# Kernel optimization log

Measured on AMD Instinct MI355X. Metric: run time of the kernel, lower is better.

The kernel has to match this reference:

```python
import jax, jax.numpy as jnp
import numpy as np

NUM_EMBEDDINGS = 8192
EMBEDDING_DIM = 256
COMMITMENT_COST = 0.25


def setup_inputs() -> dict:
    key = jax.random.key(0)
    k1, k2 = jax.random.split(key)
    inputs = jax.random.normal(k1, (32, EMBEDDING_DIM, 1024), dtype=jnp.float32)
    # matches nn.Embedding init: uniform(-1/K, 1/K)
    scale = 1.0 / NUM_EMBEDDINGS
    weight = jax.random.uniform(k2, (NUM_EMBEDDINGS, EMBEDDING_DIM),
                                minval=-scale, maxval=scale, dtype=jnp.float32)
    return {"inputs": inputs, "weight": weight}


def reference(inputs, weight):
    # inputs: [B, D, T] -> [B, T, D]
    x = jnp.transpose(inputs, (0, 2, 1))
    B, T, D = x.shape
    flat = x.reshape(-1, D)  # [N, D]
    # squared-L2 distances to each codeword: [N, K]
    distances = (jnp.sum(flat ** 2, axis=1, keepdims=True)
                 + jnp.sum(weight ** 2, axis=1)
                 - 2.0 * flat @ weight.T)
    encoding_indices = jnp.argmin(distances, axis=1)  # [N]
    # one-hot @ weight is just a gather
    quantized = weight[encoding_indices].reshape(x.shape)  # [B, T, D]
    # straight-through estimator
    quantized_ste = x + jax.lax.stop_gradient(quantized - x)
    e_latent_loss = jnp.mean((jax.lax.stop_gradient(quantized_ste) - x) ** 2)
    q_latent_loss = jnp.mean((quantized_ste - jax.lax.stop_gradient(x)) ** 2)
    loss = q_latent_loss + COMMITMENT_COST * e_latent_loss
    quantized_out = jnp.transpose(quantized_ste, (0, 2, 1))  # [B, D, T]
    return loss, quantized_out, encoding_indices[:, None]
```

## Files before the change

### kernel.cpp

```cpp
#include <hip/hip_runtime.h>
#include <hip/hip_bf16.h>

#define Bn 32
#define Dd 256
#define Tt 1024
#define Nn (Bn * Tt)
#define Kk 8192

typedef __attribute__((ext_vector_type(8))) short bf16x8;
typedef __attribute__((ext_vector_type(4))) float f32x4;

static __device__ __forceinline__ short f2bf(float v) {
    __hip_bfloat16 h = __float2bfloat16(v);
    return *reinterpret_cast<short*>(&h);
}

#define OFF_XT    0ULL
#define OFF_XBT   33554432ULL
#define OFF_WBT   50331648ULL
#define OFF_CM    54525952ULL
#define OFF_LIST  71303168ULL
#define OFF_KEYS  75497472ULL
#define OFF_SW2   75759616ULL
#define OFF_CN    75792384ULL
#define OFF_CNT   75923456ULL
#define OFF_PART  75923712ULL
#define WS_NEED   75927808ULL
#define OFF_MASK  OFF_XBT

__global__ void k_xprep(const float* __restrict__ x, float* __restrict__ xT,
                        short* __restrict__ xbt) {
    __shared__ float tile[32][33];
    const int b = blockIdx.z, d0 = blockIdx.y * 32, t0 = blockIdx.x * 32;
    const int tx = threadIdx.x, ty = threadIdx.y;
#pragma unroll
    for (int r = 0; r < 32; r += 8)
        tile[ty + r][tx] = x[((size_t)(b * Dd + d0 + ty + r)) * Tt + t0 + tx];
    __syncthreads();
#pragma unroll
    for (int r = 0; r < 32; r += 8) {
        const size_t o = (size_t)(b * Tt + t0 + ty + r) * Dd + d0 + tx;
        const float v = tile[tx][ty + r];
        xT[o] = v;
        xbt[o] = f2bf(v);
    }
}

__global__ void k_wbf(const float* __restrict__ w, short* __restrict__ wbt) {
    const int i = (blockIdx.x * 256 + threadIdx.x) * 4;
    const float4 v = *reinterpret_cast<const float4*>(&w[i]);
    short4 o;
    o.x = f2bf(v.x); o.y = f2bf(v.y); o.z = f2bf(v.z); o.w = f2bf(v.w);
    *reinterpret_cast<short4*>(&wbt[i]) = o;
}

__global__ void k_sumx2_np(const float* __restrict__ x, float* __restrict__ c) {
#pragma clang fp contract(off)
    const int n = blockIdx.x * 256 + threadIdx.x;
    const int b = n >> 10, t = n & 1023;
    const float* p = x + (size_t)b * (Dd * Tt) + t;
    float h[2];
#pragma unroll
    for (int half = 0; half < 2; ++half) {
        float r[8];
#pragma unroll
        for (int j = 0; j < 8; ++j) {
            const float v = p[(size_t)(half * 128 + j) * Tt];
            r[j] = v * v;
        }
        for (int i = 8; i < 128; i += 8) {
#pragma unroll
            for (int j = 0; j < 8; ++j) {
                const float v = p[(size_t)(half * 128 + i + j) * Tt];
                const float sq = v * v;
                r[j] = r[j] + sq;
            }
        }
        h[half] = ((r[0] + r[1]) + (r[2] + r[3])) + ((r[4] + r[5]) + (r[6] + r[7]));
    }
    c[n] = h[0] + h[1];
}

__global__ void k_sumw2_np(const float* __restrict__ w, float* __restrict__ sw) {
#pragma clang fp contract(off)
    const int k = blockIdx.x * 256 + threadIdx.x;
    const float* p = w + (size_t)k * Dd;
    float h[2];
#pragma unroll
    for (int half = 0; half < 2; ++half) {
        float r[8];
#pragma unroll
        for (int j = 0; j < 8; ++j) {
            const float v = p[half * 128 + j];
            r[j] = v * v;
        }
        for (int i = 8; i < 128; i += 8) {
#pragma unroll
            for (int j = 0; j < 8; ++j) {
                const float v = p[half * 128 + i + j];
                const float sq = v * v;
                r[j] = r[j] + sq;
            }
        }
        h[half] = ((r[0] + r[1]) + (r[2] + r[3])) + ((r[4] + r[5]) + (r[6] + r[7]));
    }
    sw[k] = h[0] + h[1];
}

__global__ void __launch_bounds__(512, 4)
k_mfma_filter(const short* __restrict__ xbt, const short* __restrict__ wbt,
              const float* __restrict__ sw2, float* __restrict__ cm) {
    __shared__ __align__(16) short Ws[128 * 264];
    const int tid = threadIdx.x;
    const int n0 = blockIdx.x * 128;
    const int cbase = blockIdx.y * 32;
    const int wid = tid >> 6, lane = tid & 63;
    const int rp = wid >> 1, cp = wid & 1;
    const int l15 = lane & 15, l4 = lane >> 4;

    bf16x8 a[2][8];
#pragma unroll
    for (int rt = 0; rt < 2; ++rt)
#pragma unroll
        for (int ks = 0; ks < 8; ++ks)
            a[rt][ks] = *reinterpret_cast<const bf16x8*>(
                &xbt[(size_t)(n0 + 32 * rp + 16 * rt + l15) * Dd + 32 * ks + 8 * l4]);

    for (int cc = 0; cc < 32; ++cc) {
        const int c = cbase + cc;
#pragma unroll
        for (int m = 0; m < 8; ++m) {
            const int e = tid + 512 * m;
            const int code = e >> 5, d8 = e & 31;
            *reinterpret_cast<bf16x8*>(&Ws[code * 264 + 8 * d8]) =
                *reinterpret_cast<const bf16x8*>(
                    &wbt[(size_t)(128 * c + code) * Dd + 8 * d8]);
        }
        __syncthreads();

        f32x4 acc[2][4];
#pragma unroll
        for (int rt = 0; rt < 2; ++rt)
#pragma unroll
            for (int ct = 0; ct < 4; ++ct) acc[rt][ct] = (f32x4)0.0f;

#pragma unroll
        for (int ks = 0; ks < 8; ++ks) {
            bf16x8 b[4];
#pragma unroll
            for (int ct = 0; ct < 4; ++ct)
                b[ct] = *reinterpret_cast<const bf16x8*>(
                    &Ws[(64 * cp + 16 * ct + l15) * 264 + 32 * ks + 8 * l4]);
#pragma unroll
            for (int rt = 0; rt < 2; ++rt)
#pragma unroll
                for (int ct = 0; ct < 4; ++ct)
                    acc[rt][ct] = __builtin_amdgcn_mfma_f32_16x16x32_bf16(
                        a[rt][ks], b[ct], acc[rt][ct], 0, 0, 0);
        }
        __syncthreads();

        float swc[4];
#pragma unroll
        for (int ct = 0; ct < 4; ++ct)
            swc[ct] = sw2[128 * c + 64 * cp + 16 * ct + l15];
#pragma unroll
        for (int rt = 0; rt < 2; ++rt) {
#pragma unroll
            for (int r = 0; r < 4; ++r) {
                float mm = fmaf(-2.0f, acc[rt][0][r], swc[0]);
#pragma unroll
                for (int ct = 1; ct < 4; ++ct)
                    mm = fminf(mm, fmaf(-2.0f, acc[rt][ct][r], swc[ct]));
#pragma unroll
                for (int d = 1; d < 16; d <<= 1)
                    mm = fminf(mm, __shfl_xor(mm, d));
                if (l15 == 0) {
                    const int row = n0 + 32 * rp + 16 * rt + 4 * l4 + r;
                    cm[(size_t)row * 128 + 2 * c + cp] = mm;
                }
            }
        }
    }
}

__global__ void __launch_bounds__(256)
k_mask(const float* __restrict__ cm, const float* __restrict__ cn,
       unsigned long long* __restrict__ mask, unsigned long long* __restrict__ keys) {
    const int tid = threadIdx.x;
    const int lane = tid & 63, w = tid >> 6;
    const int grp = lane >> 4, sub = lane & 15;
    const int n0 = blockIdx.x * 256;
    for (int pass = 0; pass < 16; ++pass) {
        const int row = n0 + pass * 16 + 4 * w + grp;
        const float4 v0 = *reinterpret_cast<const float4*>(&cm[(size_t)row * 128 + 8 * sub]);
        const float4 v1 = *reinterpret_cast<const float4*>(&cm[(size_t)row * 128 + 8 * sub + 4]);
        float gmin = fminf(fminf(fminf(v0.x, v0.y), fminf(v0.z, v0.w)),
                           fminf(fminf(v1.x, v1.y), fminf(v1.z, v1.w)));
#pragma unroll
        for (int m = 1; m < 16; m <<= 1) gmin = fminf(gmin, __shfl_xor(gmin, m));
        const float margin = 7.1e-5f + 2.6e-5f * sqrtf(cn[row]);
        const float thr = gmin + margin;
        unsigned int nib = 0;
        if (fminf(v0.x, v0.y) <= thr) nib |= 1u;
        if (fminf(v0.z, v0.w) <= thr) nib |= 2u;
        if (fminf(v1.x, v1.y) <= thr) nib |= 4u;
        if (fminf(v1.z, v1.w) <= thr) nib |= 8u;
        unsigned long long mk = (unsigned long long)nib << (4 * sub);
#pragma unroll
        for (int m = 1; m < 16; m <<= 1) mk |= __shfl_xor(mk, m);
        if (sub == 0) {
            mask[row] = mk;
            keys[row] = 0xFFFFFFFFFFFFFFFFULL;
        }
    }
}

__global__ void __launch_bounds__(1024)
k_compact(const unsigned long long* __restrict__ mask,
          unsigned int* __restrict__ cnt, unsigned short* __restrict__ lists) {
    __shared__ unsigned int sc[1024];
    const int c = blockIdx.x;
    const int t = threadIdx.x;
    const int r0 = t * 32;
    unsigned int word = 0;
#pragma unroll
    for (int j = 0; j < 32; ++j)
        word |= (unsigned int)((mask[r0 + j] >> c) & 1ULL) << j;
    const unsigned int mycnt = __popc(word);
    sc[t] = mycnt;
    __syncthreads();
    for (int off = 1; off < 1024; off <<= 1) {
        const unsigned int v = sc[t];
        const unsigned int add = (t >= off) ? sc[t - off] : 0u;
        __syncthreads();
        sc[t] = v + add;
        __syncthreads();
    }
    unsigned int base = sc[t] - mycnt;
    unsigned short* lc = lists + (size_t)c * Nn;
    unsigned int wrd = word;
    while (wrd) {
        const int j = __ffs(wrd) - 1;
        lc[base++] = (unsigned short)(r0 + j);
        wrd &= wrd - 1;
    }
    if (t == 1023) cnt[c] = sc[1023];
}

#define NGB 8
__global__ void __launch_bounds__(256, 1)
k_refine(const float* __restrict__ xT, const float* __restrict__ w,
         const float* __restrict__ sw2, const float* __restrict__ cn,
         const unsigned int* __restrict__ cnt, const unsigned short* __restrict__ lists,
         unsigned long long* __restrict__ keys) {
    __shared__ __align__(16) float xs[64 * 260];
    __shared__ __align__(16) float ws[128 * 68];
    __shared__ float cns[64];
    __shared__ unsigned short rid_s[64];
    const int c = blockIdx.x, gb = blockIdx.y;
    const int tid = threadIdx.x;
    const int cntc = (int)cnt[c];
    const int kl = tid & 31, rg = tid >> 5;
    float swk[4];
#pragma unroll
    for (int cc = 0; cc < 4; ++cc) swk[cc] = sw2[128 * c + kl + 32 * cc];

    for (int start = gb * 64; start < cntc; start += NGB * 64) {
#pragma unroll
        for (int m = 0; m < 16; ++m) {
            const int e = tid + 256 * m;
            const int j = e >> 6, d4 = e & 63;
            const int li = min(start + j, cntc - 1);
            const int row = lists[(size_t)c * Nn + li];
            *reinterpret_cast<float4*>(&xs[j * 260 + 4 * d4]) =
                *reinterpret_cast<const float4*>(&xT[(size_t)row * Dd + 4 * d4]);
        }
        if (tid < 64) {
            const int li = min(start + tid, cntc - 1);
            const unsigned short row = lists[(size_t)c * Nn + li];
            rid_s[tid] = row;
            cns[tid] = cn[row];
        }
        __syncthreads();

        float acc[8][4];
#pragma unroll
        for (int rr = 0; rr < 8; ++rr)
#pragma unroll
            for (int cc = 0; cc < 4; ++cc) acc[rr][cc] = 0.0f;

        for (int step = 0; step < 4; ++step) {
#pragma unroll
            for (int m = 0; m < 8; ++m) {
                const int e = tid + 256 * m;
                const int code = e >> 4, dseg = e & 15;
                *reinterpret_cast<float4*>(&ws[code * 68 + 4 * dseg]) =
                    *reinterpret_cast<const float4*>(
                        &w[(size_t)(128 * c + code) * Dd + step * 64 + 4 * dseg]);
            }
            __syncthreads();
#pragma unroll
            for (int dl = 0; dl < 16; ++dl) {
                float4 wv[4];
#pragma unroll
                for (int cc = 0; cc < 4; ++cc)
                    wv[cc] = *reinterpret_cast<const float4*>(
                        &ws[(kl + 32 * cc) * 68 + 4 * dl]);
#pragma unroll
                for (int rr = 0; rr < 8; ++rr) {
                    const float4 xv = *reinterpret_cast<const float4*>(
                        &xs[(8 * rg + rr) * 260 + step * 64 + 4 * dl]);
#pragma unroll
                    for (int cc = 0; cc < 4; ++cc) {
                        acc[rr][cc] = fmaf(xv.x, wv[cc].x, acc[rr][cc]);
                        acc[rr][cc] = fmaf(xv.y, wv[cc].y, acc[rr][cc]);
                        acc[rr][cc] = fmaf(xv.z, wv[cc].z, acc[rr][cc]);
                        acc[rr][cc] = fmaf(xv.w, wv[cc].w, acc[rr][cc]);
                    }
                }
            }
            __syncthreads();
        }

#pragma unroll
        for (int rr = 0; rr < 8; ++rr) {
            const int rl = 8 * rg + rr;
            const float cr = cns[rl];
            float bv = 3.402823466e+38f;
            int bk = 0x7FFFFFFF;
#pragma unroll
            for (int cc = 0; cc < 4; ++cc) {
                const float t1 = cr + swk[cc];
                const float s = fmaf(-2.0f, acc[rr][cc], t1);
                const int k = 128 * c + kl + 32 * cc;
                if (s < bv || (s == bv && k < bk)) { bv = s; bk = k; }
            }
#pragma unroll
            for (int d = 1; d < 32; d <<= 1) {
                const float ov = __shfl_xor(bv, d);
                const int ok = __shfl_xor(bk, d);
                if (ov < bv || (ov == bv && ok < bk)) { bv = ov; bk = ok; }
            }
            if (kl == 0) {
                const unsigned long long key =
                    ((unsigned long long)__float_as_uint(bv) << 32) |
                    (unsigned long long)(unsigned int)bk;
                atomicMin(&keys[rid_s[rl]], key);
            }
        }
        __syncthreads();
    }
}

__global__ void k_quant2(const float* __restrict__ x, const float* __restrict__ w,
                         const unsigned long long* __restrict__ keys,
                         float* __restrict__ outq, float* __restrict__ idxf,
                         double* __restrict__ part) {
#pragma clang fp contract(off)
    __shared__ double red[256];
    const int tid = threadIdx.x;
    const int n0 = blockIdx.x * 64;
    const int b = n0 >> 10, t0 = n0 & 1023;
    const int tl = tid & 63;
    const int d0 = tid >> 6;
    const int n = n0 + tl;
    const int code = (int)(unsigned int)(keys[n] & 0xFFFFFFFFULL);
    if (tid < 64) idxf[n0 + tid] = (float)(int)(unsigned int)(keys[n0 + tid] & 0xFFFFFFFFULL);
    const float* wr = w + (size_t)code * Dd;
    const size_t base = (size_t)b * (Dd * Tt) + t0 + tl;
    double s = 0.0;
    for (int d = d0; d < Dd; d += 4) {
        const float xv = x[base + (size_t)d * Tt];
        const float qv = wr[d];
        const float d1 = qv - xv;
        const float qs = xv + d1;
        const float d2 = qs - xv;
        s += (double)d2 * (double)d2;
        outq[base + (size_t)d * Tt] = qs;
    }
    red[tid] = s;
    __syncthreads();
    for (int st = 128; st > 0; st >>= 1) {
        if (tid < st) red[tid] += red[tid + st];
        __syncthreads();
    }
    if (tid == 0) part[blockIdx.x] = red[0];
}

__global__ void k_loss(const double* __restrict__ part, float* __restrict__ loss) {
    __shared__ double red[512];
    const int tid = threadIdx.x;
    red[tid] = part[tid];
    __syncthreads();
    for (int st = 256; st > 0; st >>= 1) {
        if (tid < st) red[tid] += red[tid + st];
        __syncthreads();
    }
    if (tid == 0)
        loss[0] = (float)(1.25 * red[0] / (double)((size_t)Bn * Dd * Tt));
}

__global__ void k_transpose(const float* __restrict__ w, float* __restrict__ wtg) {
    __shared__ float tile[32][33];
    const int k0 = blockIdx.x * 32;
    const int d0 = blockIdx.y * 32;
    const int tx = threadIdx.x, ty = threadIdx.y;
#pragma unroll
    for (int r = 0; r < 32; r += 8)
        tile[r + ty][tx] = w[(size_t)(k0 + r + ty) * Dd + d0 + tx];
    __syncthreads();
#pragma unroll
    for (int r = 0; r < 32; r += 8)
        wtg[(size_t)(d0 + r + ty) * Kk + k0 + tx] = tile[tx][r + ty];
}

template <bool WTG>
__global__ void __launch_bounds__(512, 2)
k_argmin(const float* __restrict__ x, const float* __restrict__ w,
         const float* __restrict__ wtg, const float* __restrict__ sw2,
         const float* __restrict__ cn,
         int* __restrict__ idx_out, float* __restrict__ idx_f) {
    __shared__ __align__(16) float At[32][132];
    __shared__ __align__(16) float Wt[32][268];
    const int tid = threadIdx.x;
    const int n0 = blockIdx.x * 128;
    const int b = n0 >> 10;
    const int t0 = n0 & 1023;
    const int ty = tid >> 5;
    const int tx = tid & 31;
    const int r0 = ty * 4;
    const int c0 = tx * 4;
    const float* xb = x + (size_t)b * (Dd * Tt) + t0;

    float c8[8];
#pragma unroll
    for (int i = 0; i < 8; ++i) {
        const int row = (i < 4) ? (r0 + i) : (64 + r0 + (i - 4));
        c8[i] = cn[n0 + row];
    }
    float best[8];
    int bidx[8];
#pragma unroll
    for (int i = 0; i < 8; ++i) { best[i] = 3.402823466e+38f; bidx[i] = 0; }

    for (int kc = 0; kc < Kk; kc += 256) {
        float acc[8][8];
#pragma unroll
        for (int i = 0; i < 8; ++i)
#pragma unroll
            for (int j = 0; j < 8; ++j) acc[i][j] = 0.0f;
        for (int ds = 0; ds < Dd; ds += 32) {
#pragma unroll
            for (int u = 0; u < 2; ++u) {
                int cc = tid + 512 * u;
                int dd = cc >> 5, i4 = cc & 31;
                float4 v = *reinterpret_cast<const float4*>(
                    &xb[(size_t)(ds + dd) * Tt + i4 * 4]);
                *reinterpret_cast<float4*>(&At[dd][i4 * 4]) = v;
            }
            if (WTG) {
#pragma unroll
                for (int u = 0; u < 4; ++u) {
                    int cc = tid + 512 * u;
                    int dd = cc >> 6, j4 = cc & 63;
                    float4 v = *reinterpret_cast<const float4*>(
                        &wtg[(size_t)(ds + dd) * Kk + kc + j4 * 4]);
                    *reinterpret_cast<float4*>(&Wt[dd][j4 * 4]) = v;
                }
            } else {
#pragma unroll
                for (int u = 0; u < 4; ++u) {
                    int cc = tid + 512 * u;
                    int j = cc >> 3, m = cc & 7;
                    float4 v = *reinterpret_cast<const float4*>(
                        &w[(size_t)(kc + j) * Dd + ds + m * 4]);
                    Wt[m * 4 + 0][j] = v.x;
                    Wt[m * 4 + 1][j] = v.y;
                    Wt[m * 4 + 2][j] = v.z;
                    Wt[m * 4 + 3][j] = v.w;
                }
            }
            __syncthreads();
#pragma unroll 8
            for (int dd = 0; dd < 32; ++dd) {
                float4 a0 = *reinterpret_cast<const float4*>(&At[dd][r0]);
                float4 a1 = *reinterpret_cast<const float4*>(&At[dd][64 + r0]);
                float4 b0 = *reinterpret_cast<const float4*>(&Wt[dd][c0]);
                float4 b1 = *reinterpret_cast<const float4*>(&Wt[dd][128 + c0]);
                float av[8] = {a0.x, a0.y, a0.z, a0.w, a1.x, a1.y, a1.z, a1.w};
                float bv[8] = {b0.x, b0.y, b0.z, b0.w, b1.x, b1.y, b1.z, b1.w};
#pragma unroll
                for (int i = 0; i < 8; ++i)
#pragma unroll
                    for (int j = 0; j < 8; ++j)
                        acc[i][j] = fmaf(av[i], bv[j], acc[i][j]);
            }
            __syncthreads();
        }
#pragma unroll
        for (int j = 0; j < 8; ++j) {
            const int col = (j < 4) ? (c0 + j) : (128 + c0 + (j - 4));
            const int k = kc + col;
            const float sw = sw2[k];
#pragma unroll
            for (int i = 0; i < 8; ++i) {
                const float t1 = c8[i] + sw;
                const float s = fmaf(-2.0f, acc[i][j], t1);
                if (s < best[i] || (s == best[i] && k < bidx[i])) {
                    best[i] = s; bidx[i] = k;
                }
            }
        }
    }
#pragma unroll
    for (int i = 0; i < 8; ++i) {
        float v = best[i];
        int id = bidx[i];
#pragma unroll
        for (int m = 1; m < 32; m <<= 1) {
            const float ov = __shfl_xor(v, m);
            const int oi = __shfl_xor(id, m);
            if (ov < v || (ov == v && oi < id)) { v = ov; id = oi; }
        }
        if (tx == 0) {
            const int row = (i < 4) ? (r0 + i) : (64 + r0 + (i - 4));
            const int n = n0 + row;
            idx_out[n] = id;
            idx_f[n] = (float)id;
        }
    }
}

__global__ void k_quant(const float* __restrict__ x, const float* __restrict__ w,
                        const int* __restrict__ idx, float* __restrict__ outq,
                        double* __restrict__ part) {
#pragma clang fp contract(off)
    __shared__ double red[256];
    const int tid = threadIdx.x;
    const int n0 = blockIdx.x * 64;
    const int b = n0 >> 10, t0 = n0 & 1023;
    const int tl = tid & 63;
    const int d0 = tid >> 6;
    const int n = n0 + tl;
    const int code = idx[n];
    const float* wr = w + (size_t)code * Dd;
    const size_t base = (size_t)b * (Dd * Tt) + t0 + tl;
    double s = 0.0;
    for (int d = d0; d < Dd; d += 4) {
        const float xv = x[base + (size_t)d * Tt];
        const float qv = wr[d];
        const float d1 = qv - xv;
        const float qs = xv + d1;
        const float d2 = qs - xv;
        s += (double)d2 * (double)d2;
        outq[base + (size_t)d * Tt] = qs;
    }
    red[tid] = s;
    __syncthreads();
    for (int st = 128; st > 0; st >>= 1) {
        if (tid < st) red[tid] += red[tid + st];
        __syncthreads();
    }
    if (tid == 0) part[blockIdx.x] = red[0];
}

extern "C" void kernel_launch(void* const* d_in, const int* in_sizes, int n_in,
                              void* d_out, int out_size, void* d_ws, size_t ws_size,
                              hipStream_t stream) {
    const float* x = (const float*)d_in[0];
    const float* w = (const float*)d_in[1];
    float* out = (float*)d_out;
    float* loss = out;
    float* outq = out + 1;
    float* idxf = out + 1 + (size_t)Bn * Dd * Tt;
    char* ws = (char*)d_ws;

    if (ws_size >= WS_NEED) {
        float* xT = (float*)(ws + OFF_XT);
        short* xbt = (short*)(ws + OFF_XBT);
        short* wbt = (short*)(ws + OFF_WBT);
        float* cm = (float*)(ws + OFF_CM);
        unsigned long long* mask = (unsigned long long*)(ws + OFF_MASK);
        unsigned short* lists = (unsigned short*)(ws + OFF_LIST);
        unsigned long long* keys = (unsigned long long*)(ws + OFF_KEYS);
        float* sw2 = (float*)(ws + OFF_SW2);
        float* cn = (float*)(ws + OFF_CN);
        unsigned int* cnt = (unsigned int*)(ws + OFF_CNT);
        double* part = (double*)(ws + OFF_PART);

        k_xprep<<<dim3(32, 8, 32), dim3(32, 8), 0, stream>>>(x, xT, xbt);
        k_wbf<<<(Kk * Dd) / 1024, 256, 0, stream>>>(w, wbt);
        k_sumx2_np<<<Nn / 256, 256, 0, stream>>>(x, cn);
        k_sumw2_np<<<Kk / 256, 256, 0, stream>>>(w, sw2);
        k_mfma_filter<<<dim3(Nn / 128, 2), 512, 0, stream>>>(xbt, wbt, sw2, cm);
        k_mask<<<Nn / 256, 256, 0, stream>>>(cm, cn, mask, keys);
        k_compact<<<64, 1024, 0, stream>>>(mask, cnt, lists);
        k_refine<<<dim3(64, NGB), 256, 0, stream>>>(xT, w, sw2, cn, cnt, lists, keys);
        k_quant2<<<Nn / 64, 256, 0, stream>>>(x, w, keys, outq, idxf, part);
        k_loss<<<1, 512, 0, stream>>>(part, loss);
    } else {
        float* sw2 = (float*)(ws);
        int* idx = (int*)(ws + 32768);
        double* part = (double*)(ws + 163840);
        float* cn = (float*)(ws + 172032);
        float* wtg = (float*)(ws + 524288);
        const bool use_wtg = ws_size >= (size_t)524288 + (size_t)Kk * Dd * 4;
        if (use_wtg)
            k_transpose<<<dim3(Kk / 32, Dd / 32), dim3(32, 8), 0, stream>>>(w, wtg);
        k_sumx2_np<<<Nn / 256, 256, 0, stream>>>(x, cn);
        k_sumw2_np<<<Kk / 256, 256, 0, stream>>>(w, sw2);
        if (use_wtg)
            k_argmin<true><<<Nn / 128, 512, 0, stream>>>(x, w, wtg, sw2, cn, idx, idxf);
        else
            k_argmin<false><<<Nn / 128, 512, 0, stream>>>(x, w, wtg, sw2, cn, idx, idxf);
        k_quant<<<Nn / 64, 256, 0, stream>>>(x, w, idx, outq, part);
        k_loss<<<1, 512, 0, stream>>>(part, loss);
    }
}
```

Measured before the change: 441.0 us.

## Retile MFMA filter to 64-row blocks and reduce per-128-code minima in-kernel

The bf16 MFMA filter now uses 256-thread blocks covering 64 input rows, with each wave owning 32 codes across all rows instead of a row/column split. Per-wave minima are combined through shared memory into one minimum per 128-code chunk, so the cm buffer is halved. The mask kernel then reads one float per group instead of pairing two. The aim is to cut cm write/read traffic and the per-thread reduction work. The cost is twice as many W tile loads per row, more A-fragment registers, and an extra barrier per chunk; sumx2 also moves to 128-thread blocks while the fallback path keeps a legacy copy.

```diff
diff --git a/kernel.cpp b/kernel.cpp
--- a/kernel.cpp
+++ b/kernel.cpp
@@ -56,7 +56,7 @@
 
 __global__ void k_sumx2_np(const float* __restrict__ x, float* __restrict__ c) {
 #pragma clang fp contract(off)
-    const int n = blockIdx.x * 256 + threadIdx.x;
+    const int n = blockIdx.x * 128 + threadIdx.x;
     const int b = n >> 10, t = n & 1023;
     const float* p = x + (size_t)b * (Dd * Tt) + t;
     float h[2];
@@ -107,30 +107,30 @@
     sw[k] = h[0] + h[1];
 }
 
-__global__ void __launch_bounds__(512, 4)
+__global__ void __launch_bounds__(256, 2)
 k_mfma_filter(const short* __restrict__ xbt, const short* __restrict__ wbt,
               const float* __restrict__ sw2, float* __restrict__ cm) {
     __shared__ __align__(16) short Ws[128 * 264];
+    __shared__ float red[64][4];
     const int tid = threadIdx.x;
-    const int n0 = blockIdx.x * 128;
+    const int n0 = blockIdx.x * 64;
     const int cbase = blockIdx.y * 32;
-    const int wid = tid >> 6, lane = tid & 63;
-    const int rp = wid >> 1, cp = wid & 1;
-    const int l15 = lane & 15, l4 = lane >> 4;
-
-    bf16x8 a[2][8];
-#pragma unroll
-    for (int rt = 0; rt < 2; ++rt)
+    const int wv = tid >> 6, ln = tid & 63;
+    const int l15 = ln & 15, l4 = ln >> 4;
+
+    bf16x8 a[4][8];
+#pragma unroll
+    for (int rt = 0; rt < 4; ++rt)
 #pragma unroll
         for (int ks = 0; ks < 8; ++ks)
             a[rt][ks] = *reinterpret_cast<const bf16x8*>(
-                &xbt[(size_t)(n0 + 32 * rp + 16 * rt + l15) * Dd + 32 * ks + 8 * l4]);
+                &xbt[(size_t)(n0 + 16 * rt + l15) * Dd + 32 * ks + 8 * l4]);
 
     for (int cc = 0; cc < 32; ++cc) {
         const int c = cbase + cc;
 #pragma unroll
-        for (int m = 0; m < 8; ++m) {
-            const int e = tid + 512 * m;
+        for (int m = 0; m < 16; ++m) {
+            const int e = tid + 256 * m;
             const int code = e >> 5, d8 = e & 31;
             *reinterpret_cast<bf16x8*>(&Ws[code * 264 + 8 * d8]) =
                 *reinterpret_cast<const bf16x8*>(
@@ -138,48 +138,49 @@
         }
         __syncthreads();
 
-        f32x4 acc[2][4];
-#pragma unroll
-        for (int rt = 0; rt < 2; ++rt)
-#pragma unroll
-            for (int ct = 0; ct < 4; ++ct) acc[rt][ct] = (f32x4)0.0f;
+        f32x4 acc[4][2];
+#pragma unroll
+        for (int rt = 0; rt < 4; ++rt)
+#pragma unroll
+            for (int ct = 0; ct < 2; ++ct) acc[rt][ct] = (f32x4)0.0f;
 
 #pragma unroll
         for (int ks = 0; ks < 8; ++ks) {
-            bf16x8 b[4];
-#pragma unroll
-            for (int ct = 0; ct < 4; ++ct)
+            bf16x8 b[2];
+#pragma unroll
+            for (int ct = 0; ct < 2; ++ct)
                 b[ct] = *reinterpret_cast<const bf16x8*>(
-                    &Ws[(64 * cp + 16 * ct + l15) * 264 + 32 * ks + 8 * l4]);
-#pragma unroll
-            for (int rt = 0; rt < 2; ++rt)
-#pragma unroll
-                for (int ct = 0; ct < 4; ++ct)
+                    &Ws[(32 * wv + 16 * ct + l15) * 264 + 32 * ks + 8 * l4]);
+#pragma unroll
+            for (int rt = 0; rt < 4; ++rt)
+#pragma unroll
+                for (int ct = 0; ct < 2; ++ct)
                     acc[rt][ct] = __builtin_amdgcn_mfma_f32_16x16x32_bf16(
                         a[rt][ks], b[ct], acc[rt][ct], 0, 0, 0);
         }
-        __syncthreads();
-
-        float swc[4];
-#pragma unroll
-        for (int ct = 0; ct < 4; ++ct)
-            swc[ct] = sw2[128 * c + 64 * cp + 16 * ct + l15];
-#pragma unroll
-        for (int rt = 0; rt < 2; ++rt) {
+
+        float swc[2];
+#pragma unroll
+        for (int ct = 0; ct < 2; ++ct)
+            swc[ct] = sw2[128 * c + 32 * wv + 16 * ct + l15];
+#pragma unroll
+        for (int rt = 0; rt < 4; ++rt) {
 #pragma unroll
             for (int r = 0; r < 4; ++r) {
-                float mm = fmaf(-2.0f, acc[rt][0][r], swc[0]);
-#pragma unroll
-                for (int ct = 1; ct < 4; ++ct)
-                    mm = fminf(mm, fmaf(-2.0f, acc[rt][ct][r], swc[ct]));
+                float mm = fminf(fmaf(-2.0f, acc[rt][0][r], swc[0]),
+                                 fmaf(-2.0f, acc[rt][1][r], swc[1]));
 #pragma unroll
                 for (int d = 1; d < 16; d <<= 1)
                     mm = fminf(mm, __shfl_xor(mm, d));
-                if (l15 == 0) {
-                    const int row = n0 + 32 * rp + 16 * rt + 4 * l4 + r;
-                    cm[(size_t)row * 128 + 2 * c + cp] = mm;
-                }
-            }
+                if (l15 == 0) red[16 * rt + 4 * l4 + r][wv] = mm;
+            }
+        }
+        __syncthreads();
+
+        if (tid < 64) {
+            const float mm = fminf(fminf(red[tid][0], red[tid][1]),
+                                   fminf(red[tid][2], red[tid][3]));
+            cm[(size_t)(n0 + tid) * 64 + c] = mm;
         }
     }
 }
@@ -188,24 +189,22 @@
 k_mask(const float* __restrict__ cm, const float* __restrict__ cn,
        unsigned long long* __restrict__ mask, unsigned long long* __restrict__ keys) {
     const int tid = threadIdx.x;
-    const int lane = tid & 63, w = tid >> 6;
-    const int grp = lane >> 4, sub = lane & 15;
-    const int n0 = blockIdx.x * 256;
-    for (int pass = 0; pass < 16; ++pass) {
+    const int ln = tid & 63, w = tid >> 6;
+    const int grp = ln >> 4, sub = ln & 15;
+    const int n0 = blockIdx.x * 128;
+    for (int pass = 0; pass < 8; ++pass) {
         const int row = n0 + pass * 16 + 4 * w + grp;
-        const float4 v0 = *reinterpret_cast<const float4*>(&cm[(size_t)row * 128 + 8 * sub]);
-        const float4 v1 = *reinterpret_cast<const float4*>(&cm[(size_t)row * 128 + 8 * sub + 4]);
-        float gmin = fminf(fminf(fminf(v0.x, v0.y), fminf(v0.z, v0.w)),
-                           fminf(fminf(v1.x, v1.y), fminf(v1.z, v1.w)));
+        const float4 v = *reinterpret_cast<const float4*>(&cm[(size_t)row * 64 + 4 * sub]);
+        float gmin = fminf(fminf(v.x, v.y), fminf(v.z, v.w));
 #pragma unroll
         for (int m = 1; m < 16; m <<= 1) gmin = fminf(gmin, __shfl_xor(gmin, m));
         const float margin = 7.1e-5f + 2.6e-5f * sqrtf(cn[row]);
         const float thr = gmin + margin;
         unsigned int nib = 0;
-        if (fminf(v0.x, v0.y) <= thr) nib |= 1u;
-        if (fminf(v0.z, v0.w) <= thr) nib |= 2u;
-        if (fminf(v1.x, v1.y) <= thr) nib |= 4u;
-        if (fminf(v1.z, v1.w) <= thr) nib |= 8u;
+        if (v.x <= thr) nib |= 1u;
+        if (v.y <= thr) nib |= 2u;
+        if (v.z <= thr) nib |= 4u;
+        if (v.w <= thr) nib |= 8u;
         unsigned long long mk = (unsigned long long)nib << (4 * sub);
 #pragma unroll
         for (int m = 1; m < 16; m <<= 1) mk |= __shfl_xor(mk, m);
@@ -415,6 +414,33 @@
         wtg[(size_t)(d0 + r + ty) * Kk + k0 + tx] = tile[tx][r + ty];
 }
 
+__global__ void k_sumx2_np_legacy(const float* __restrict__ x, float* __restrict__ c) {
+#pragma clang fp contract(off)
+    const int n = blockIdx.x * 256 + threadIdx.x;
+    const int b = n >> 10, t = n & 1023;
+    const float* p = x + (size_t)b * (Dd * Tt) + t;
+    float h[2];
+#pragma unroll
+    for (int half = 0; half < 2; ++half) {
+        float r[8];
+#pragma unroll
+        for (int j = 0; j < 8; ++j) {
+            const float v = p[(size_t)(half * 128 + j) * Tt];
+            r[j] = v * v;
+        }
+        for (int i = 8; i < 128; i += 8) {
+#pragma unroll
+            for (int j = 0; j < 8; ++j) {
+                const float v = p[(size_t)(half * 128 + i + j) * Tt];
+                const float sq = v * v;
+                r[j] = r[j] + sq;
+            }
+        }
+        h[half] = ((r[0] + r[1]) + (r[2] + r[3])) + ((r[4] + r[5]) + (r[6] + r[7]));
+    }
+    c[n] = h[0] + h[1];
+}
+
 template <bool WTG>
 __global__ void __launch_bounds__(512, 2)
 k_argmin(const float* __restrict__ x, const float* __restrict__ w,
@@ -591,10 +617,10 @@
 
         k_xprep<<<dim3(32, 8, 32), dim3(32, 8), 0, stream>>>(x, xT, xbt);
         k_wbf<<<(Kk * Dd) / 1024, 256, 0, stream>>>(w, wbt);
-        k_sumx2_np<<<Nn / 256, 256, 0, stream>>>(x, cn);
+        k_sumx2_np<<<Nn / 128, 128, 0, stream>>>(x, cn);
         k_sumw2_np<<<Kk / 256, 256, 0, stream>>>(w, sw2);
-        k_mfma_filter<<<dim3(Nn / 128, 2), 512, 0, stream>>>(xbt, wbt, sw2, cm);
-        k_mask<<<Nn / 256, 256, 0, stream>>>(cm, cn, mask, keys);
+        k_mfma_filter<<<dim3(Nn / 64, 2), 256, 0, stream>>>(xbt, wbt, sw2, cm);
+        k_mask<<<Nn / 128, 256, 0, stream>>>(cm, cn, mask, keys);
         k_compact<<<64, 1024, 0, stream>>>(mask, cnt, lists);
         k_refine<<<dim3(64, NGB), 256, 0, stream>>>(xT, w, sw2, cn, cnt, lists, keys);
         k_quant2<<<Nn / 64, 256, 0, stream>>>(x, w, keys, outq, idxf, part);
@@ -608,7 +634,7 @@
         const bool use_wtg = ws_size >= (size_t)524288 + (size_t)Kk * Dd * 4;
         if (use_wtg)
             k_transpose<<<dim3(Kk / 32, Dd / 32), dim3(32, 8), 0, stream>>>(w, wtg);
-        k_sumx2_np<<<Nn / 256, 256, 0, stream>>>(x, cn);
+        k_sumx2_np_legacy<<<Nn / 256, 256, 0, stream>>>(x, cn);
         k_sumw2_np<<<Kk / 256, 256, 0, stream>>>(w, sw2);
         if (use_wtg)
             k_argmin<true><<<Nn / 128, 512, 0, stream>>>(x, w, wtg, sw2, cn, idx, idxf);
```

New measurement: 580.9 us. 1.32x slower.
